# Performance work log

Hardware: AMD Instinct MI355X
Metric: run time of the kernel (lower is better)

Reference implementation:

```python
import jax, jax.numpy as jnp
import numpy as np

N = 50000      # nodes
F_IN = 2048    # raw node feature dim (pooled to 1024)
POOL = 1024
E = 1600000    # directed edges
E_SEL = 200000 # labeled edges for link prediction


def setup_inputs() -> dict:
    key = jax.random.key(0)
    ks = jax.random.split(key, 24)
    def lin(k, fin, fout):
        return jax.random.normal(k, (fin, fout), dtype=jnp.float32) / np.float32(np.sqrt(fin))
    inp = {
        "x": jax.random.normal(ks[0], (N, F_IN), dtype=jnp.float32),
        "edge_index": jax.random.randint(ks[1], (2, E), 0, N, dtype=jnp.int32),
        "mask": jax.random.randint(ks[2], (E_SEL,), 0, E, dtype=jnp.int32),
        "ln_g": jnp.ones((POOL,), jnp.float32),
        "ln_b": jnp.zeros((POOL,), jnp.float32),
        "w0": lin(ks[3], 1024, 512), "b0": jnp.zeros((512,), jnp.float32),
        "w1": lin(ks[4], 512, 128),  "b1": jnp.zeros((128,), jnp.float32),
        "w2": lin(ks[5], 128, 64),   "b2": jnp.zeros((64,), jnp.float32),
        "c1w": lin(ks[6], 64, 32),   "c1b": jnp.zeros((32,), jnp.float32),
        "c2w": lin(ks[7], 32, 16),   "c2b": jnp.zeros((16,), jnp.float32),
        "lw1": lin(ks[8], 32, 16),   "lb1": jnp.zeros((16,), jnp.float32),
        "lw2": lin(ks[9], 16, 2),    "lb2": jnp.zeros((2,), jnp.float32),
    }
    return inp


def gcn_conv(x, src, dst, W, b):
    # PyG GCNConv: add self loops, symmetric normalization D^-1/2 (A+I) D^-1/2 (x @ W) + b
    xw = x @ W
    loop = jnp.arange(N, dtype=src.dtype)
    src2 = jnp.concatenate([src, loop])
    dst2 = jnp.concatenate([dst, loop])
    deg = jax.ops.segment_sum(jnp.ones(src2.shape[0], xw.dtype), dst2, num_segments=N)
    dinv = jax.lax.rsqrt(jnp.maximum(deg, 1e-12))
    norm = dinv[src2] * dinv[dst2]              # [E+N]
    out = jax.ops.segment_sum(xw[src2] * norm[:, None], dst2, num_segments=N)
    return out + b


def reference(x, edge_index, mask, ln_g, ln_b, w0, b0, w1, b1, w2, b2,
              c1w, c1b, c2w, c2b, lw1, lb1, lw2, lb2):
    src, dst = edge_index[0], edge_index[1]
    # AdaptiveMaxPool1d(1024): exact divisor case -> max over contiguous pairs
    h = x.reshape(N, POOL, F_IN // POOL).max(axis=-1)
    # LayerNorm(1024)
    mu = h.mean(axis=-1, keepdims=True)
    var = jnp.mean(jnp.square(h - mu), axis=-1, keepdims=True)
    h = (h - mu) * jax.lax.rsqrt(var + 1e-5) * ln_g + ln_b
    h = jax.nn.elu(h @ w0 + b0)
    h = jax.nn.elu(h @ w1 + b1)
    h = jax.nn.elu(h @ w2 + b2)
    # dropout p=0.2 -> identity in eval mode
    h = jax.nn.elu(gcn_conv(h, src, dst, c1w, c1b))
    z = gcn_conv(h, src, dst, c2w, c2b)          # [N, 16]
    sel = edge_index[:, mask]                    # labeled edges
    e = jnp.concatenate([z[sel[0]], z[sel[1]]], axis=1)  # [E_SEL, 32]
    e = jax.nn.elu(e @ lw1 + lb1)
    return e @ lw2 + lb2                         # [E_SEL, 2]
```

## Files before the change

kernel.cpp:

```cpp
#include <hip/hip_runtime.h>
#include <cstdint>

using short8  = __attribute__((ext_vector_type(8))) short;
using floatx4 = __attribute__((ext_vector_type(4))) float;

__device__ __forceinline__ unsigned short f2bf(float x){
  union { float f; unsigned u; } v; v.f = x;
  unsigned r = v.u + 0x7fffu + ((v.u >> 16) & 1u);
  return (unsigned short)(r >> 16);
}

__device__ __forceinline__ float eluf(float v){ return v > 0.f ? v : expm1f(v); }

__device__ __forceinline__ void ld_g2l16(const void* g, void* l){
  __builtin_amdgcn_global_load_lds(
      (const __attribute__((address_space(1))) void*)g,
      (__attribute__((address_space(3))) void*)l, 16, 0, 0);
}

__global__ void k_tcvt(const float* __restrict__ W, unsigned short* __restrict__ Wt,
                       int K, int Ncols){
  int idx = blockIdx.x * 256 + threadIdx.x;
  if (idx >= K * Ncols) return;
  int n = idx / K, k = idx - n * K;
  Wt[idx] = f2bf(W[(size_t)k * Ncols + n]);
}

__global__ __launch_bounds__(256) void k_pool_ln(const float* __restrict__ x,
    const float* __restrict__ g, const float* __restrict__ b,
    unsigned short* __restrict__ h0){
  const int i = blockIdx.x, t = threadIdx.x;
  const float4* xr = (const float4*)(x + (size_t)i * 2048);
  float4 va = xr[2 * t], vb = xr[2 * t + 1];
  float v0 = fmaxf(va.x, va.y), v1 = fmaxf(va.z, va.w);
  float v2 = fmaxf(vb.x, vb.y), v3 = fmaxf(vb.z, vb.w);
  float s  = v0 + v1 + v2 + v3;
  float s2 = v0*v0 + v1*v1 + v2*v2 + v3*v3;
  #pragma unroll
  for (int off = 32; off > 0; off >>= 1){
    s  += __shfl_down(s, off);
    s2 += __shfl_down(s2, off);
  }
  __shared__ float ps[4], ps2[4];
  int w = t >> 6;
  if ((t & 63) == 0){ ps[w] = s; ps2[w] = s2; }
  __syncthreads();
  float S  = ps[0] + ps[1] + ps[2] + ps[3];
  float S2 = ps2[0] + ps2[1] + ps2[2] + ps2[3];
  float mu   = S * (1.f / 1024.f);
  float var  = S2 * (1.f / 1024.f) - mu * mu;
  float rstd = rsqrtf(var + 1e-5f);
  float4 g4 = ((const float4*)g)[t];
  float4 b4 = ((const float4*)b)[t];
  ushort4 o;
  o.x = f2bf((v0 - mu) * rstd * g4.x + b4.x);
  o.y = f2bf((v1 - mu) * rstd * g4.y + b4.y);
  o.z = f2bf((v2 - mu) * rstd * g4.z + b4.z);
  o.w = f2bf((v3 - mu) * rstd * g4.w + b4.w);
  *(ushort4*)(h0 + (size_t)i * 1024 + t * 4) = o;
}

__global__ __launch_bounds__(256) void k_gemm(const unsigned short* __restrict__ A,
    const unsigned short* __restrict__ Bt, const float* __restrict__ bias,
    unsigned short* __restrict__ C, int M, int K, int N){
  __shared__ __align__(16) unsigned short lA[128 * 64];
  __shared__ __align__(16) unsigned short lB[128 * 64];
  const int tid  = threadIdx.x;
  const int lane = tid & 63;
  const int w    = tid >> 6;
  const int wm = w >> 1, wn = w & 1;
  const int m0 = blockIdx.x * 128;
  const int n0 = blockIdx.y * 128;
  const int q = lane >> 4, ml = lane & 15;
  floatx4 acc[4][4] = {};
  const int nKB = K >> 6;
  for (int kb = 0; kb < nKB; ++kb){
    #pragma unroll
    for (int i = 0; i < 4; ++i){
      int cpos = (w * 4 + i) * 64 + lane;
      int row  = cpos >> 3;
      int p    = cpos & 7;
      int cc   = p ^ (row & 7);
      int ar   = m0 + row; ar = ar < M ? ar : M - 1;
      ld_g2l16(A  + (size_t)ar        * K + (kb * 64 + cc * 8), &lA[(w * 4 + i) * 512]);
      ld_g2l16(Bt + (size_t)(n0 + row) * K + (kb * 64 + cc * 8), &lB[(w * 4 + i) * 512]);
    }
    __syncthreads();
    #pragma unroll
    for (int kk = 0; kk < 2; ++kk){
      short8 af[4], bfr[4];
      #pragma unroll
      for (int mi = 0; mi < 4; ++mi){
        int row = wm * 64 + mi * 16 + ml;
        int p   = (kk * 4 + q) ^ (row & 7);
        af[mi] = *(const short8*)&lA[row * 64 + p * 8];
      }
      #pragma unroll
      for (int ni = 0; ni < 4; ++ni){
        int row = wn * 64 + ni * 16 + ml;
        int p   = (kk * 4 + q) ^ (row & 7);
        bfr[ni] = *(const short8*)&lB[row * 64 + p * 8];
      }
      #pragma unroll
      for (int mi = 0; mi < 4; ++mi)
        #pragma unroll
        for (int ni = 0; ni < 4; ++ni)
          acc[mi][ni] = __builtin_amdgcn_mfma_f32_16x16x32_bf16(af[mi], bfr[ni], acc[mi][ni], 0, 0, 0);
    }
    __syncthreads();
  }
  #pragma unroll
  for (int mi = 0; mi < 4; ++mi){
    #pragma unroll
    for (int ni = 0; ni < 4; ++ni){
      int gc = n0 + wn * 64 + ni * 16 + ml;
      float bv = bias[gc];
      #pragma unroll
      for (int r = 0; r < 4; ++r){
        int gr = m0 + wm * 64 + mi * 16 + q * 4 + r;
        if (gr < M){
          float v = acc[mi][ni][r] + bv;
          v = v > 0.f ? v : expm1f(v);
          C[(size_t)gr * N + gc] = f2bf(v);
        }
      }
    }
  }
}

__global__ __launch_bounds__(256) void k_h3(const unsigned short* __restrict__ h2,
    const unsigned short* __restrict__ w2t, const float* __restrict__ b2,
    unsigned short* __restrict__ h3, int M){
  int gw = (blockIdx.x * 256 + threadIdx.x) >> 6;
  int lane = threadIdx.x & 63;
  int r0 = gw * 16;
  if (r0 >= M) return;
  int ml = lane & 15, q = lane >> 4;
  int ar = r0 + ml; if (ar >= M) ar = M - 1;
  floatx4 acc[4] = {};
  #pragma unroll
  for (int kk = 0; kk < 4; ++kk){
    short8 a = *(const short8*)&h2[(size_t)ar * 128 + kk * 32 + q * 8];
    #pragma unroll
    for (int ni = 0; ni < 4; ++ni){
      short8 bb = *(const short8*)&w2t[(ni * 16 + ml) * 128 + kk * 32 + q * 8];
      acc[ni] = __builtin_amdgcn_mfma_f32_16x16x32_bf16(a, bb, acc[ni], 0, 0, 0);
    }
  }
  #pragma unroll
  for (int ni = 0; ni < 4; ++ni){
    int gc = ni * 16 + ml;
    float bv = b2[gc];
    #pragma unroll
    for (int r = 0; r < 4; ++r){
      int gr = r0 + q * 4 + r;
      if (gr < M) h3[(size_t)gr * 64 + gc] = f2bf(eluf(acc[ni][r] + bv));
    }
  }
}

__global__ __launch_bounds__(256) void k_xs1(const unsigned short* __restrict__ h3,
    const unsigned short* __restrict__ c1wt, const float* __restrict__ dinv,
    float* __restrict__ xs1, float* __restrict__ acc1, int M){
  int gw = (blockIdx.x * 256 + threadIdx.x) >> 6;
  int lane = threadIdx.x & 63;
  int r0 = gw * 16;
  if (r0 >= M) return;
  int ml = lane & 15, q = lane >> 4;
  int ar = r0 + ml; if (ar >= M) ar = M - 1;
  floatx4 acc[2] = {};
  #pragma unroll
  for (int kk = 0; kk < 2; ++kk){
    short8 a = *(const short8*)&h3[(size_t)ar * 64 + kk * 32 + q * 8];
    #pragma unroll
    for (int ni = 0; ni < 2; ++ni){
      short8 bb = *(const short8*)&c1wt[(ni * 16 + ml) * 64 + kk * 32 + q * 8];
      acc[ni] = __builtin_amdgcn_mfma_f32_16x16x32_bf16(a, bb, acc[ni], 0, 0, 0);
    }
  }
  #pragma unroll
  for (int ni = 0; ni < 2; ++ni){
    int gc = ni * 16 + ml;
    #pragma unroll
    for (int r = 0; r < 4; ++r){
      int gr = r0 + q * 4 + r;
      if (gr < M){
        float v = acc[ni][r] * dinv[gr];
        xs1[(size_t)gr * 32 + gc]  = v;
        acc1[(size_t)gr * 32 + gc] = v;
      }
    }
  }
}

__global__ __launch_bounds__(256) void k_fin1(const float* __restrict__ acc1,
    const float* __restrict__ c1b, const unsigned short* __restrict__ c2wt,
    const float* __restrict__ dinv, float* __restrict__ xs2,
    float* __restrict__ acc2, int M){
  int gw = (blockIdx.x * 256 + threadIdx.x) >> 6;
  int lane = threadIdx.x & 63;
  int r0 = gw * 16;
  if (r0 >= M) return;
  int ml = lane & 15, q = lane >> 4;
  int ar = r0 + ml; if (ar >= M) ar = M - 1;
  float dr = dinv[ar];
  short8 a;
  #pragma unroll
  for (int j = 0; j < 8; ++j){
    float v = dr * acc1[(size_t)ar * 32 + q * 8 + j] + c1b[q * 8 + j];
    a[j] = (short)f2bf(eluf(v));
  }
  short8 bb = *(const short8*)&c2wt[ml * 32 + q * 8];
  floatx4 c = {0.f, 0.f, 0.f, 0.f};
  c = __builtin_amdgcn_mfma_f32_16x16x32_bf16(a, bb, c, 0, 0, 0);
  #pragma unroll
  for (int r = 0; r < 4; ++r){
    int gr = r0 + q * 4 + r;
    if (gr < M){
      float v = c[r] * dinv[gr];
      xs2[(size_t)gr * 16 + ml]  = v;
      acc2[(size_t)gr * 16 + ml] = v;
    }
  }
}

__global__ void k_deg_init(float* __restrict__ deg, int Nn){
  int i = blockIdx.x * 256 + threadIdx.x;
  if (i < Nn) deg[i] = 1.0f;
}
__global__ void k_deg_count(const int* __restrict__ ei, float* __restrict__ deg, int E){
  int e = blockIdx.x * 256 + threadIdx.x;
  if (e < E) atomicAdd(&deg[ei[E + e]], 1.0f);
}
__global__ void k_dinv(const float* __restrict__ deg, float* __restrict__ dinv, int Nn){
  int i = blockIdx.x * 256 + threadIdx.x;
  if (i < Nn) dinv[i] = rsqrtf(deg[i]);
}

__global__ void k_scat32(const int* __restrict__ ei, const float* __restrict__ xs,
                         float* __restrict__ acc, int E){
  int gid = blockIdx.x * 256 + threadIdx.x;
  int e = gid >> 5, c = gid & 31;
  if (e >= E) return;
  int s = ei[e], d = ei[E + e];
  atomicAdd(&acc[(size_t)d * 32 + c], xs[(size_t)s * 32 + c]);
}
__global__ void k_scat16(const int* __restrict__ ei, const float* __restrict__ xs,
                         float* __restrict__ acc, int E){
  int gid = blockIdx.x * 256 + threadIdx.x;
  int e = gid >> 4, c = gid & 15;
  if (e >= E) return;
  int s = ei[e], d = ei[E + e];
  atomicAdd(&acc[(size_t)d * 16 + c], xs[(size_t)s * 16 + c]);
}

__global__ void k_fin2(const float* __restrict__ acc2, const float* __restrict__ c2b,
                       const float* __restrict__ dinv, float* __restrict__ z, int M){
  int gid = blockIdx.x * 256 + threadIdx.x;
  if (gid >= M * 16) return;
  int i = gid >> 4, c = gid & 15;
  z[gid] = dinv[i] * acc2[gid] + c2b[c];
}

__global__ __launch_bounds__(256) void k_edge(const int* __restrict__ ei,
    const int* __restrict__ mask, const float* __restrict__ z,
    const float* __restrict__ lw1, const float* __restrict__ lb1,
    const float* __restrict__ lw2, const float* __restrict__ lb2,
    float* __restrict__ out, int nsel, int E){
  __shared__ float w1s[512], b1s[16], w2s[32], b2s[2];
  int t = threadIdx.x;
  for (int idx = t; idx < 512; idx += 256) w1s[idx] = lw1[idx];
  if (t < 16) b1s[t] = lb1[t];
  if (t < 32) w2s[t] = lw2[t];
  if (t < 2)  b2s[t] = lb2[t];
  __syncthreads();
  int j = blockIdx.x * 256 + t;
  if (j >= nsel) return;
  int m = mask[j];
  int s = ei[m], d = ei[E + m];
  float e[32];
  const float4* zs = (const float4*)(z + (size_t)s * 16);
  const float4* zd = (const float4*)(z + (size_t)d * 16);
  #pragma unroll
  for (int k4 = 0; k4 < 4; ++k4){
    float4 v = zs[k4];
    e[k4 * 4 + 0] = v.x; e[k4 * 4 + 1] = v.y; e[k4 * 4 + 2] = v.z; e[k4 * 4 + 3] = v.w;
  }
  #pragma unroll
  for (int k4 = 0; k4 < 4; ++k4){
    float4 v = zd[k4];
    e[16 + k4 * 4 + 0] = v.x; e[16 + k4 * 4 + 1] = v.y;
    e[16 + k4 * 4 + 2] = v.z; e[16 + k4 * 4 + 3] = v.w;
  }
  float o[16];
  #pragma unroll
  for (int oo = 0; oo < 16; ++oo){
    float acc = b1s[oo];
    #pragma unroll
    for (int ii = 0; ii < 32; ++ii) acc += e[ii] * w1s[ii * 16 + oo];
    o[oo] = eluf(acc);
  }
  float r0 = b2s[0], r1 = b2s[1];
  #pragma unroll
  for (int oo = 0; oo < 16; ++oo){ r0 += o[oo] * w2s[oo * 2]; r1 += o[oo] * w2s[oo * 2 + 1]; }
  out[(size_t)j * 2]     = r0;
  out[(size_t)j * 2 + 1] = r1;
}

extern "C" void kernel_launch(void* const* d_in, const int* in_sizes, int n_in,
                              void* d_out, int out_size, void* d_ws, size_t ws_size,
                              hipStream_t stream){
  const float* x    = (const float*)d_in[0];
  const int*   ei   = (const int*)d_in[1];
  const int*   mask = (const int*)d_in[2];
  const float* ln_g = (const float*)d_in[3];
  const float* ln_b = (const float*)d_in[4];
  const float* w0   = (const float*)d_in[5];
  const float* b0   = (const float*)d_in[6];
  const float* w1   = (const float*)d_in[7];
  const float* b1   = (const float*)d_in[8];
  const float* w2   = (const float*)d_in[9];
  const float* b2   = (const float*)d_in[10];
  const float* c1w  = (const float*)d_in[11];
  const float* c1b  = (const float*)d_in[12];
  const float* c2w  = (const float*)d_in[13];
  const float* c2b  = (const float*)d_in[14];
  const float* lw1  = (const float*)d_in[15];
  const float* lb1  = (const float*)d_in[16];
  const float* lw2  = (const float*)d_in[17];
  const float* lb2  = (const float*)d_in[18];
  float* out = (float*)d_out;

  const int N    = in_sizes[0] / 2048;
  const int E    = in_sizes[1] / 2;
  const int NSEL = in_sizes[2];

  char* ws = (char*)d_ws;
  size_t o = 0;
  unsigned short* h2   = (unsigned short*)(ws + o); o += (size_t)N * 256;
  float* xs1  = (float*)(ws + o); o += (size_t)N * 128;
  float* acc1 = (float*)(ws + o); o += (size_t)N * 128;
  float* xs2  = (float*)(ws + o); o += (size_t)N * 64;
  float* acc2 = (float*)(ws + o); o += (size_t)N * 64;
  float* z    = (float*)(ws + o); o += (size_t)N * 64;
  float* deg  = (float*)(ws + o); o += (size_t)N * 4;
  float* dinv = (float*)(ws + o); o += (size_t)N * 4;
  unsigned short* h3 = (unsigned short*)(ws + o);
  unsigned short* h0 = (unsigned short*)(ws + 0);
  size_t base2 = (size_t)N * 2048;
  unsigned short* h1   = (unsigned short*)(ws + base2);        o = base2 + (size_t)N * 1024;
  unsigned short* w0t  = (unsigned short*)(ws + o);            o += 1024 * 512 * 2;
  unsigned short* w1t  = (unsigned short*)(ws + o);            o += 512 * 128 * 2;
  unsigned short* w2t  = (unsigned short*)(ws + o);            o += 128 * 64 * 2;
  unsigned short* c1wt = (unsigned short*)(ws + o);            o += 64 * 32 * 2;
  unsigned short* c2wt = (unsigned short*)(ws + o);

  k_tcvt<<<(1024 * 512 + 255) / 256, 256, 0, stream>>>(w0, w0t, 1024, 512);
  k_tcvt<<<(512 * 128 + 255) / 256, 256, 0, stream>>>(w1, w1t, 512, 128);
  k_tcvt<<<(128 * 64 + 255) / 256, 256, 0, stream>>>(w2, w2t, 128, 64);
  k_tcvt<<<(64 * 32 + 255) / 256, 256, 0, stream>>>(c1w, c1wt, 64, 32);
  k_tcvt<<<(32 * 16 + 255) / 256, 256, 0, stream>>>(c2w, c2wt, 32, 16);

  k_pool_ln<<<N, 256, 0, stream>>>(x, ln_g, ln_b, h0);

  k_gemm<<<dim3((N + 127) / 128, 4), 256, 0, stream>>>(h0, w0t, b0, h1, N, 1024, 512);

  k_deg_init<<<(N + 255) / 256, 256, 0, stream>>>(deg, N);
  k_deg_count<<<(E + 255) / 256, 256, 0, stream>>>(ei, deg, E);
  k_dinv<<<(N + 255) / 256, 256, 0, stream>>>(deg, dinv, N);

  k_gemm<<<dim3((N + 127) / 128, 1), 256, 0, stream>>>(h1, w1t, b1, h2, N, 512, 128);

  int nwaves = (N + 15) / 16;
  int wblocks = (nwaves + 3) / 4;
  k_h3<<<wblocks, 256, 0, stream>>>(h2, w2t, b2, h3, N);

  k_xs1<<<wblocks, 256, 0, stream>>>(h3, c1wt, dinv, xs1, acc1, N);
  k_scat32<<<((size_t)E * 32 + 255) / 256, 256, 0, stream>>>(ei, xs1, acc1, E);
  k_fin1<<<wblocks, 256, 0, stream>>>(acc1, c1b, c2wt, dinv, xs2, acc2, N);

  k_scat16<<<((size_t)E * 16 + 255) / 256, 256, 0, stream>>>(ei, xs2, acc2, E);
  k_fin2<<<(N * 16 + 255) / 256, 256, 0, stream>>>(acc2, c2b, dinv, z, N);

  k_edge<<<(NSEL + 255) / 256, 256, 0, stream>>>(ei, mask, z, lw1, lb1, lw2, lb2,
                                                 out, NSEL, E);
}
```

Before: 1.105 ms.

## Replace atomic edge scatter with CSR build and per-node wave gather

Builds a destination-sorted CSR adjacency each call (integer degree count, block scan, atomic fill) and replaces the per-element float atomicAdd scatters for both GCN layers with per-node wavefront gathers using float4 loads and shuffle reductions. The aim is to remove about 77M float atomics on the accumulation buffers and the duplicate acc initialisation writes. In exchange it adds several small launches, a second pass over the edge list, and nondeterministic neighbour order inside each CSR row.

```diff
diff --git a/kernel.cpp b/kernel.cpp
--- a/kernel.cpp
+++ b/kernel.cpp
@@ -161,7 +161,7 @@
 
 __global__ __launch_bounds__(256) void k_xs1(const unsigned short* __restrict__ h3,
     const unsigned short* __restrict__ c1wt, const float* __restrict__ dinv,
-    float* __restrict__ xs1, float* __restrict__ acc1, int M){
+    float* __restrict__ xs1, int M){
   int gw = (blockIdx.x * 256 + threadIdx.x) >> 6;
   int lane = threadIdx.x & 63;
   int r0 = gw * 16;
@@ -184,19 +184,14 @@
     #pragma unroll
     for (int r = 0; r < 4; ++r){
       int gr = r0 + q * 4 + r;
-      if (gr < M){
-        float v = acc[ni][r] * dinv[gr];
-        xs1[(size_t)gr * 32 + gc]  = v;
-        acc1[(size_t)gr * 32 + gc] = v;
-      }
+      if (gr < M) xs1[(size_t)gr * 32 + gc] = acc[ni][r] * dinv[gr];
     }
   }
 }
 
 __global__ __launch_bounds__(256) void k_fin1(const float* __restrict__ acc1,
     const float* __restrict__ c1b, const unsigned short* __restrict__ c2wt,
-    const float* __restrict__ dinv, float* __restrict__ xs2,
-    float* __restrict__ acc2, int M){
+    const float* __restrict__ dinv, float* __restrict__ xs2, int M){
   int gw = (blockIdx.x * 256 + threadIdx.x) >> 6;
   int lane = threadIdx.x & 63;
   int r0 = gw * 16;
@@ -216,42 +211,92 @@
   #pragma unroll
   for (int r = 0; r < 4; ++r){
     int gr = r0 + q * 4 + r;
-    if (gr < M){
-      float v = c[r] * dinv[gr];
-      xs2[(size_t)gr * 16 + ml]  = v;
-      acc2[(size_t)gr * 16 + ml] = v;
-    }
-  }
-}
-
-__global__ void k_deg_init(float* __restrict__ deg, int Nn){
+    if (gr < M) xs2[(size_t)gr * 16 + ml] = c[r] * dinv[gr];
+  }
+}
+
+__global__ void k_zero2(int* __restrict__ a, int* __restrict__ b, int Nn){
   int i = blockIdx.x * 256 + threadIdx.x;
-  if (i < Nn) deg[i] = 1.0f;
-}
-__global__ void k_deg_count(const int* __restrict__ ei, float* __restrict__ deg, int E){
+  if (i < Nn){ a[i] = 0; b[i] = 0; }
+}
+__global__ void k_degi(const int* __restrict__ ei, int* __restrict__ deg, int E){
   int e = blockIdx.x * 256 + threadIdx.x;
-  if (e < E) atomicAdd(&deg[ei[E + e]], 1.0f);
-}
-__global__ void k_dinv(const float* __restrict__ deg, float* __restrict__ dinv, int Nn){
+  if (e < E) atomicAdd(&deg[ei[E + e]], 1);
+}
+__global__ void k_dinv(const int* __restrict__ deg, float* __restrict__ dinv, int Nn){
   int i = blockIdx.x * 256 + threadIdx.x;
-  if (i < Nn) dinv[i] = rsqrtf(deg[i]);
-}
-
-__global__ void k_scat32(const int* __restrict__ ei, const float* __restrict__ xs,
-                         float* __restrict__ acc, int E){
-  int gid = blockIdx.x * 256 + threadIdx.x;
-  int e = gid >> 5, c = gid & 31;
+  if (i < Nn) dinv[i] = rsqrtf((float)deg[i] + 1.0f);
+}
+__global__ __launch_bounds__(256) void k_scan1(const int* __restrict__ deg,
+    int* __restrict__ ptr, int* __restrict__ btot, int Nn){
+  __shared__ int s[256];
+  int b = blockIdx.x, t = threadIdx.x, i = b * 256 + t;
+  int v = (i < Nn) ? deg[i] : 0;
+  s[t] = v; __syncthreads();
+  #pragma unroll
+  for (int off = 1; off < 256; off <<= 1){
+    int x = (t >= off) ? s[t - off] : 0;
+    __syncthreads();
+    s[t] += x; __syncthreads();
+  }
+  if (i < Nn) ptr[i] = s[t] - v;
+  if (t == 255) btot[b] = s[255];
+}
+__global__ __launch_bounds__(256) void k_scan2(int* __restrict__ btot, int nb){
+  __shared__ int s[256];
+  int t = threadIdx.x;
+  int v = (t < nb) ? btot[t] : 0;
+  s[t] = v; __syncthreads();
+  #pragma unroll
+  for (int off = 1; off < 256; off <<= 1){
+    int x = (t >= off) ? s[t - off] : 0;
+    __syncthreads();
+    s[t] += x; __syncthreads();
+  }
+  if (t < nb) btot[t] = s[t] - v;
+}
+__global__ void k_scan3(int* __restrict__ ptr, const int* __restrict__ btot, int Nn){
+  int i = blockIdx.x * 256 + threadIdx.x;
+  if (i < Nn) ptr[i] += btot[blockIdx.x >> 0 ? i >> 8 : 0];
+}
+__global__ void k_fill(const int* __restrict__ ei, const int* __restrict__ ptr,
+                       int* __restrict__ cnt, int* __restrict__ csr, int E){
+  int e = blockIdx.x * 256 + threadIdx.x;
   if (e >= E) return;
-  int s = ei[e], d = ei[E + e];
-  atomicAdd(&acc[(size_t)d * 32 + c], xs[(size_t)s * 32 + c]);
-}
-__global__ void k_scat16(const int* __restrict__ ei, const float* __restrict__ xs,
-                         float* __restrict__ acc, int E){
-  int gid = blockIdx.x * 256 + threadIdx.x;
-  int e = gid >> 4, c = gid & 15;
-  if (e >= E) return;
-  int s = ei[e], d = ei[E + e];
-  atomicAdd(&acc[(size_t)d * 16 + c], xs[(size_t)s * 16 + c]);
+  int d = ei[E + e];
+  int pos = ptr[d] + atomicAdd(&cnt[d], 1);
+  csr[pos] = ei[e];
+}
+
+template <int C4, int LOG2C4>
+__global__ __launch_bounds__(256) void k_gather(const int* __restrict__ csr,
+    const int* __restrict__ ptr, const int* __restrict__ deg,
+    const float* __restrict__ xs, float* __restrict__ acc, int M){
+  int wid = (blockIdx.x * 256 + threadIdx.x) >> 6;
+  if (wid >= M) return;
+  int lane = threadIdx.x & 63;
+  int g = lane >> LOG2C4;
+  int c = lane & (C4 - 1);
+  const int EPI = 64 >> LOG2C4;
+  int start = ptr[wid], n = deg[wid];
+  float4 a = {0.f, 0.f, 0.f, 0.f};
+  for (int j = g; j < n; j += EPI){
+    int s = csr[start + j];
+    float4 v = *(const float4*)&xs[(size_t)s * (C4 * 4) + c * 4];
+    a.x += v.x; a.y += v.y; a.z += v.z; a.w += v.w;
+  }
+  #pragma unroll
+  for (int off = C4; off < 64; off <<= 1){
+    a.x += __shfl_xor(a.x, off);
+    a.y += __shfl_xor(a.y, off);
+    a.z += __shfl_xor(a.z, off);
+    a.w += __shfl_xor(a.w, off);
+  }
+  if (g == 0){
+    float4 self = *(const float4*)&xs[(size_t)wid * (C4 * 4) + c * 4];
+    float4 o = {a.x + self.x, a.y + self.y, a.z + self.z, a.w + self.w};
+    *(float4*)&acc[(size_t)wid * (C4 * 4) + c * 4] = o;
+  }
 }
 
 __global__ void k_fin2(const float* __restrict__ acc2, const float* __restrict__ c2b,
@@ -334,6 +379,7 @@
   const int N    = in_sizes[0] / 2048;
   const int E    = in_sizes[1] / 2;
   const int NSEL = in_sizes[2];
+  const int NB   = (N + 255) / 256;
 
   char* ws = (char*)d_ws;
   size_t o = 0;
@@ -343,9 +389,13 @@
   float* xs2  = (float*)(ws + o); o += (size_t)N * 64;
   float* acc2 = (float*)(ws + o); o += (size_t)N * 64;
   float* z    = (float*)(ws + o); o += (size_t)N * 64;
-  float* deg  = (float*)(ws + o); o += (size_t)N * 4;
+  int*   degi = (int*)(ws + o);   o += (size_t)N * 4;
   float* dinv = (float*)(ws + o); o += (size_t)N * 4;
-  unsigned short* h3 = (unsigned short*)(ws + o);
+  int*   ptr  = (int*)(ws + o);   o += (size_t)N * 4;
+  int*   cnt  = (int*)(ws + o);   o += (size_t)N * 4;
+  int*   btot = (int*)(ws + o);   o += 256 * 4;
+  int*   csr  = (int*)(ws + o);   o += (size_t)E * 4;
+  unsigned short* h3 = (unsigned short*)(ws + o);   o += (size_t)N * 128;
   unsigned short* h0 = (unsigned short*)(ws + 0);
   size_t base2 = (size_t)N * 2048;
   unsigned short* h1   = (unsigned short*)(ws + base2);        o = base2 + (size_t)N * 1024;
@@ -365,9 +415,13 @@
 
   k_gemm<<<dim3((N + 127) / 128, 4), 256, 0, stream>>>(h0, w0t, b0, h1, N, 1024, 512);
 
-  k_deg_init<<<(N + 255) / 256, 256, 0, stream>>>(deg, N);
-  k_deg_count<<<(E + 255) / 256, 256, 0, stream>>>(ei, deg, E);
-  k_dinv<<<(N + 255) / 256, 256, 0, stream>>>(deg, dinv, N);
+  k_zero2<<<NB, 256, 0, stream>>>(degi, cnt, N);
+  k_degi<<<(E + 255) / 256, 256, 0, stream>>>(ei, degi, E);
+  k_dinv<<<NB, 256, 0, stream>>>(degi, dinv, N);
+  k_scan1<<<NB, 256, 0, stream>>>(degi, ptr, btot, N);
+  k_scan2<<<1, 256, 0, stream>>>(btot, NB);
+  k_scan3<<<NB, 256, 0, stream>>>(ptr, btot, N);
+  k_fill<<<(E + 255) / 256, 256, 0, stream>>>(ei, ptr, cnt, csr, E);
 
   k_gemm<<<dim3((N + 127) / 128, 1), 256, 0, stream>>>(h1, w1t, b1, h2, N, 512, 128);
 
@@ -375,11 +429,11 @@
   int wblocks = (nwaves + 3) / 4;
   k_h3<<<wblocks, 256, 0, stream>>>(h2, w2t, b2, h3, N);
 
-  k_xs1<<<wblocks, 256, 0, stream>>>(h3, c1wt, dinv, xs1, acc1, N);
-  k_scat32<<<((size_t)E * 32 + 255) / 256, 256, 0, stream>>>(ei, xs1, acc1, E);
-  k_fin1<<<wblocks, 256, 0, stream>>>(acc1, c1b, c2wt, dinv, xs2, acc2, N);
-
-  k_scat16<<<((size_t)E * 16 + 255) / 256, 256, 0, stream>>>(ei, xs2, acc2, E);
+  k_xs1<<<wblocks, 256, 0, stream>>>(h3, c1wt, dinv, xs1, N);
+  k_gather<8, 3><<<(N + 3) / 4, 256, 0, stream>>>(csr, ptr, degi, xs1, acc1, N);
+  k_fin1<<<wblocks, 256, 0, stream>>>(acc1, c1b, c2wt, dinv, xs2, N);
+
+  k_gather<4, 2><<<(N + 3) / 4, 256, 0, stream>>>(csr, ptr, degi, xs2, acc2, N);
   k_fin2<<<(N * 16 + 255) / 256, 256, 0, stream>>>(acc2, c2b, dinv, z, N);
 
   k_edge<<<(NSEL + 255) / 256, 256, 0, stream>>>(ei, mask, z, lw1, lb1, lw2, lb2,
```

After: 974.1 us. -11.9%, faster.
